# Performance work log

Hardware: AMD Instinct MI355X
Metric: run time of the kernel (lower is better)

Reference implementation:

```python
import jax, jax.numpy as jnp
import numpy as np
import math

B, N, D, H = 2, 64, 256, 8
DK = D // H


def setup_inputs() -> dict:
    key = jax.random.key(0)
    ks = jax.random.split(key, 12)
    s = 1.0 / math.sqrt(D)
    inp = {
        "state": jax.random.normal(ks[0], (B, N, N, D), dtype=jnp.float32),
        "mask": jnp.zeros((B, N, N, N), dtype=bool),
        "W_lk": jax.random.normal(ks[1], (D, D), dtype=jnp.float32) * s,
        "b_lk": jnp.zeros((D,), dtype=jnp.float32),
        "W_rk": jax.random.normal(ks[2], (D, D), dtype=jnp.float32) * s,
        "b_rk": jnp.zeros((D,), dtype=jnp.float32),
        "W_lv": jax.random.normal(ks[3], (D, D), dtype=jnp.float32) * s,
        "b_lv": jnp.zeros((D,), dtype=jnp.float32),
        "W_rv": jax.random.normal(ks[4], (D, D), dtype=jnp.float32) * s,
        "b_rv": jnp.zeros((D,), dtype=jnp.float32),
        "W_o": jax.random.normal(ks[5], (D, D), dtype=jnp.float32) * s,
        "b_o": jnp.zeros((D,), dtype=jnp.float32),
    }
    return inp


def _proj(x, W, b):
    # torch nn.Linear: x @ W.T + b, then view to heads
    y = jnp.einsum('bxyd,ed->bxye', x, W) + b
    return y.reshape(B, N, N, H, DK)


def reference(state, mask, W_lk, b_lk, W_rk, b_rk, W_lv, b_lv, W_rv, b_rv, W_o, b_o):
    left_k = _proj(state, W_lk, b_lk)   # [B,N,N,H,DK]
    right_k = _proj(state, W_rk, b_rk)
    left_v = _proj(state, W_lv, b_lv)
    right_v = _proj(state, W_rv, b_rv)

    # triangle-style scores over node triples (x, a, y): [B,N,N,N,H]
    scores = jnp.einsum('bxahd,bayhd->bxayh', left_k, right_k) / math.sqrt(DK)
    scores = jnp.where(mask[..., None], jnp.float32(-1000.0), scores)
    att = jax.nn.softmax(scores, axis=2)  # softmax over intermediate node a

    # val[b,x,a,y,h,d] = left_v[b,x,a,h,d] * right_v[b,a,y,h,d] (materialized as in torch)
    val = jnp.einsum('bxahd,bayhd->bxayhd', left_v, right_v)
    x = jnp.einsum('bxayh,bxayhd->bxyhd', att, val)  # sum over a
    x = x.reshape(B, N, N, D)
    return jnp.einsum('bxyd,ed->bxye', x, W_o) + b_o
```

## Files before the change

### kernel.cpp

```cpp
#include <hip/hip_runtime.h>

#define B 2
#define N 64
#define D 256
#define H 8
#define DK 32
#define M (B * N * N)

typedef __attribute__((ext_vector_type(8))) short bf16x8;
typedef __attribute__((ext_vector_type(4))) float f32x4;

#define PROJ_ELEMS (2097152)

__device__ __forceinline__ ushort f2b(float f) {
    union { float f; unsigned u; } v; v.f = f;
    unsigned r = v.u + 0x7fffu + ((v.u >> 16) & 1u);
    return (ushort)(r >> 16);
}
__device__ __forceinline__ float b2f(ushort u) {
    union { unsigned u; float f; } v; v.u = ((unsigned)u) << 16; return v.f;
}
__device__ __forceinline__ void cvt8(float4 raw, float* f) {
    const ushort* s = (const ushort*)&raw;
#pragma unroll
    for (int j = 0; j < 8; ++j) f[j] = b2f(s[j]);
}

__device__ __forceinline__ void glds16(const ushort* g, ushort* l) {
    __builtin_amdgcn_global_load_lds(
        (const __attribute__((address_space(1))) unsigned int*)g,
        (__attribute__((address_space(3))) unsigned int*)l, 16, 0, 0);
}

__global__ __launch_bounds__(256) void cast_all(const float* __restrict__ state,
                                                const float* __restrict__ W_lk, const float* __restrict__ W_rk,
                                                const float* __restrict__ W_lv, const float* __restrict__ W_rv,
                                                const float* __restrict__ W_o,
                                                const float* __restrict__ b_lk, const float* __restrict__ b_rk,
                                                const float* __restrict__ b_lv, const float* __restrict__ b_rv,
                                                const float* __restrict__ b_o,
                                                ushort* __restrict__ state_bf,
                                                ushort* __restrict__ Wcat,
                                                float* __restrict__ bias_cat) {
    const int gid = blockIdx.x * 256 + threadIdx.x;
    const float* Ws[5] = {W_lk, W_rk, W_lv, W_rv, W_o};
    const float* bs[5] = {b_lk, b_rk, b_lv, b_rv, b_o};

    if (gid < 1280) bias_cat[gid] = bs[gid >> 8][gid & 255];

    if (gid < 524288) {
        float4 v = *(const float4*)&state[(size_t)gid * 4];
        ushort4 o = {f2b(v.x), f2b(v.y), f2b(v.z), f2b(v.w)};
        *(ushort4*)&state_bf[(size_t)gid * 4] = o;
    } else {
        int u = gid - 524288;
        int row = u >> 6;
        int k4 = (u & 63) * 4;
        const float* W = Ws[row >> 8];
        float4 v = *(const float4*)&W[(size_t)(row & 255) * 256 + k4];
        ushort4 o = {f2b(v.x), f2b(v.y), f2b(v.z), f2b(v.w)};
        *(ushort4*)&Wcat[(size_t)row * 256 + k4] = o;
    }
}

template <int BF16OUT, int RELAYOUT>
__global__ __launch_bounds__(256) void gemm_mfma(const ushort* __restrict__ A,
                                                 const ushort* __restrict__ Bw,
                                                 const float* __restrict__ bias,
                                                 void* __restrict__ Cv, int ldc) {
    __shared__ __align__(16) ushort As[128 * 32];
    __shared__ __align__(16) ushort Bs[128 * 32];
    const int tid = threadIdx.x;
    const int lane = tid & 63;
    const int wave = tid >> 6;
    const int wm = (wave & 1) * 64;
    const int wn = (wave >> 1) * 64;
    const int row0 = blockIdx.x * 128;
    const int col0 = blockIdx.y * 128;

    const int lr = lane >> 2;
    const int lkq = (lane & 3) * 8;

    const ushort* gA0 = A + (size_t)(row0 + wave * 32 + lr) * 256 + lkq;
    const ushort* gA1 = gA0 + 16 * 256;
    const ushort* gB0 = Bw + (size_t)(col0 + wave * 32 + lr) * 256 + lkq;
    const ushort* gB1 = gB0 + 16 * 256;
    ushort* lA0 = &As[(wave * 32) * 32];
    ushort* lA1 = &As[(wave * 32 + 16) * 32];
    ushort* lB0 = &Bs[(wave * 32) * 32];
    ushort* lB1 = &Bs[(wave * 32 + 16) * 32];

    const int fr = lane & 15;
    const int fk = (lane >> 4) * 8;

    f32x4 acc[4][4] = {};

    for (int k0 = 0; k0 < 256; k0 += 32) {
        __syncthreads();
        glds16(gA0 + k0, lA0);
        glds16(gA1 + k0, lA1);
        glds16(gB0 + k0, lB0);
        glds16(gB1 + k0, lB1);
        __syncthreads();

        bf16x8 af[4], bf[4];
#pragma unroll
        for (int i = 0; i < 4; ++i)
            af[i] = *(const bf16x8*)&As[(wm + i * 16 + fr) * 32 + fk];
#pragma unroll
        for (int j = 0; j < 4; ++j)
            bf[j] = *(const bf16x8*)&Bs[(wn + j * 16 + fr) * 32 + fk];
#pragma unroll
        for (int i = 0; i < 4; ++i)
#pragma unroll
            for (int j = 0; j < 4; ++j)
                acc[i][j] = __builtin_amdgcn_mfma_f32_16x16x32_bf16(af[i], bf[j], acc[i][j], 0, 0, 0);
    }

#pragma unroll
    for (int j = 0; j < 4; ++j) {
        const int col = col0 + wn + j * 16 + (lane & 15);
        const float bv = bias[col];
#pragma unroll
        for (int i = 0; i < 4; ++i) {
            const int rbase = row0 + wm + i * 16 + (lane >> 4) * 4;
#pragma unroll
            for (int r = 0; r < 4; ++r) {
                float o = acc[i][j][r] + bv;
                if (RELAYOUT) {
                    const int row = rbase + r;
                    const int bb = row >> 12, rr = row & 4095;
                    const int proj = col >> 8, hh = (col >> 5) & 7, dk = col & 31;
                    ((ushort*)Cv)[(size_t)proj * PROJ_ELEMS +
                                  ((size_t)(bb * 8 + hh) * 4096 + rr) * 32 + dk] = f2b(o);
                } else if (BF16OUT) {
                    ((ushort*)Cv)[(size_t)(rbase + r) * ldc + col] = f2b(o);
                } else {
                    ((float*)Cv)[(size_t)(rbase + r) * ldc + col] = o;
                }
            }
        }
    }
}

__global__ __launch_bounds__(512) void fused_attn(const ushort* __restrict__ P,
                                                  const unsigned char* __restrict__ mask,
                                                  ushort* __restrict__ xbuf) {
    __shared__ __align__(16) float LVs[16 * 16 * 44];
    __shared__ __align__(16) float RVs[16 * 16 * 44];
    __shared__ __align__(16) float atts[16 * 16 * 20];
    __shared__ float mstate[16 * 20];
    __shared__ float lstate[16 * 20];
    __shared__ float alphas[16 * 20];

    const int bh = blockIdx.z;
    const int b = bh >> 3, h = bh & 7;
    const int x0 = blockIdx.x * 16, y0 = blockIdx.y * 16;
    const int tid = threadIdx.x;
    const int lane = tid & 63, wave = tid >> 6;

    const size_t HB = (size_t)bh * 4096 * 32;
    const ushort* PLK = P + HB;
    const ushort* PRK = P + (size_t)1 * PROJ_ELEMS + HB;
    const ushort* PLV = P + (size_t)2 * PROJ_ELEMS + HB;
    const ushort* PRV = P + (size_t)3 * PROJ_ELEMS + HB;

    const int y2 = (tid >> 4) & 3, dp = tid & 15;
    const int sx = tid >> 4, sy = tid & 15;
    if (tid < 256) {
        mstate[sx * 20 + sy] = -3.0e38f;
        lstate[sx * 20 + sy] = 0.0f;
    }

    float2 acc[2][4] = {};
    const float scale = 0.17677669529663687f;

    for (int ac = 0; ac < N; ac += 16) {
        __syncthreads();
#pragma unroll
        for (int it = 0; it < 2; ++it) {
            const int row = (tid >> 2) + it * 128;
            const int q = tid & 3;
            const int a = row >> 4, r = row & 15;
            float f[8];
            cvt8(*(const float4*)&PLV[((size_t)(x0 + r) * 64 + ac + a) * 32 + q * 8], f);
            *(float4*)&LVs[row * 44 + q * 8]     = make_float4(f[0], f[1], f[2], f[3]);
            *(float4*)&LVs[row * 44 + q * 8 + 4] = make_float4(f[4], f[5], f[6], f[7]);
            cvt8(*(const float4*)&PRV[((size_t)(ac + a) * 64 + y0 + r) * 32 + q * 8], f);
            *(float4*)&RVs[row * 44 + q * 8]     = make_float4(f[0], f[1], f[2], f[3]);
            *(float4*)&RVs[row * 44 + q * 8 + 4] = make_float4(f[4], f[5], f[6], f[7]);
        }
        {
            const int fr = lane & 15, fk = (lane >> 4) * 8;
            const int yq = lane & 15, xq = (lane >> 4) * 4;
#pragma unroll
            for (int aw = 0; aw < 2; ++aw) {
                const int a = wave * 2 + aw;
                bf16x8 af = *(const bf16x8*)&PLK[((size_t)(x0 + fr) * 64 + ac + a) * 32 + fk];
                bf16x8 bf = *(const bf16x8*)&PRK[((size_t)(ac + a) * 64 + y0 + fr) * 32 + fk];
                f32x4 s = {};
                s = __builtin_amdgcn_mfma_f32_16x16x32_bf16(af, bf, s, 0, 0, 0);
#pragma unroll
                for (int rr = 0; rr < 4; ++rr) {
                    const int x = xq + rr;
                    float sv = s[rr] * scale;
                    if (mask[((size_t)(b * N + x0 + x) * N + ac + a) * N + y0 + yq]) sv = -1000.0f;
                    atts[(a * 16 + x) * 20 + yq] = sv;
                }
            }
        }
        __syncthreads();

        if (tid < 256) {
            float s16[16];
            float mc = -3.0e38f;
#pragma unroll
            for (int a = 0; a < 16; ++a) {
                s16[a] = atts[(a * 16 + sx) * 20 + sy];
                mc = fmaxf(mc, s16[a]);
            }
            const float mold = mstate[sx * 20 + sy];
            const float mnew = fmaxf(mold, mc);
            const float alpha = __expf(mold - mnew);
            float ps = 0.0f;
#pragma unroll
            for (int a = 0; a < 16; ++a) {
                float p = __expf(s16[a] - mnew);
                atts[(a * 16 + sx) * 20 + sy] = p;
                ps += p;
            }
            lstate[sx * 20 + sy] = lstate[sx * 20 + sy] * alpha + ps;
            mstate[sx * 20 + sy] = mnew;
            alphas[sx * 20 + sy] = alpha;
        }
        __syncthreads();

#pragma unroll
        for (int i = 0; i < 2; ++i) {
            const int x = wave * 2 + i;
            float4 av = *(const float4*)&alphas[x * 20 + y2 * 4];
            const float* ap = (const float*)&av;
#pragma unroll
            for (int j = 0; j < 4; ++j) {
                acc[i][j].x *= ap[j];
                acc[i][j].y *= ap[j];
            }
        }
#pragma unroll
        for (int a = 0; a < 16; ++a) {
            float2 lv[2], rv[4];
#pragma unroll
            for (int i = 0; i < 2; ++i)
                lv[i] = *(const float2*)&LVs[(a * 16 + wave * 2 + i) * 44 + dp * 2];
#pragma unroll
            for (int j = 0; j < 4; ++j)
                rv[j] = *(const float2*)&RVs[(a * 16 + y2 * 4 + j) * 44 + dp * 2];
#pragma unroll
            for (int i = 0; i < 2; ++i) {
                float4 wv = *(const float4*)&atts[(a * 16 + wave * 2 + i) * 20 + y2 * 4];
                const float* wp = (const float*)&wv;
#pragma unroll
                for (int j = 0; j < 4; ++j) {
                    acc[i][j].x += (wp[j] * lv[i].x) * rv[j].x;
                    acc[i][j].y += (wp[j] * lv[i].y) * rv[j].y;
                }
            }
        }
    }

#pragma unroll
    for (int i = 0; i < 2; ++i) {
        const int x = wave * 2 + i;
        float4 lq = *(const float4*)&lstate[x * 20 + y2 * 4];
        const float* lp = (const float*)&lq;
#pragma unroll
        for (int j = 0; j < 4; ++j) {
            const float il = 1.0f / lp[j];
            ushort2 o = {f2b(acc[i][j].x * il), f2b(acc[i][j].y * il)};
            *(ushort2*)&xbuf[(((size_t)b * N + x0 + x) * N + y0 + y2 * 4 + j) * D + h * DK + 2 * dp] = o;
        }
    }
}

extern "C" void kernel_launch(void* const* d_in, const int* in_sizes, int n_in,
                              void* d_out, int out_size, void* d_ws, size_t ws_size,
                              hipStream_t stream) {
    const float* state = (const float*)d_in[0];
    const unsigned char* mask = (const unsigned char*)d_in[1];
    const float* W_lk = (const float*)d_in[2];
    const float* b_lk = (const float*)d_in[3];
    const float* W_rk = (const float*)d_in[4];
    const float* b_rk = (const float*)d_in[5];
    const float* W_lv = (const float*)d_in[6];
    const float* b_lv = (const float*)d_in[7];
    const float* W_rv = (const float*)d_in[8];
    const float* b_rv = (const float*)d_in[9];
    const float* W_o = (const float*)d_in[10];
    const float* b_o = (const float*)d_in[11];
    float* out = (float*)d_out;

    char* ws = (char*)d_ws;
    ushort* P_bf = (ushort*)ws;
    ws += (size_t)4 * PROJ_ELEMS * 2;
    float* bias_cat = (float*)ws;
    ws += 1280 * 4;
    ushort* state_bf = (ushort*)ws;
    ws += (size_t)M * D * 2;
    ushort* Wcat = (ushort*)ws;
    ws += (size_t)1280 * 256 * 2;
    ushort* xbuf_bf = (ushort*)ws;

    cast_all<<<2368, 256, 0, stream>>>(state, W_lk, W_rk, W_lv, W_rv, W_o,
                                       b_lk, b_rk, b_lv, b_rv, b_o,
                                       state_bf, Wcat, bias_cat);
    gemm_mfma<1, 1><<<dim3(M / 128, 8), 256, 0, stream>>>(state_bf, Wcat, bias_cat, P_bf, 1024);
    fused_attn<<<dim3(4, 4, B * H), 512, 0, stream>>>(P_bf, mask, xbuf_bf);
    gemm_mfma<0, 0><<<dim3(M / 128, 2), 256, 0, stream>>>(xbuf_bf, Wcat + 1024 * 256, bias_cat + 1024, out, 256);
}
```

Measured before the change: 124.5 us.

## Split fused attention across head-dim halves and keep V tiles in bf16 LDS

The fused attention kernel now launches twice as many blocks of 256 threads, each handling one half of the 32-wide head dimension, so 512 blocks are spread over the GPU instead of 256. The left and right value tiles are stored in LDS as raw bf16 and unpacked on read, which halves their shared memory and removes the conversion step at load time. The cost is that every block recomputes the full QK scores and softmax for its tile, doubling that work, plus extra unpacking instructions in the inner loop.

Measured after the change: 123.8 us. No clear change (-0.6%).

```diff
diff --git a/kernel.cpp b/kernel.cpp
--- a/kernel.cpp
+++ b/kernel.cpp
@@ -19,6 +19,12 @@
 }
 __device__ __forceinline__ float b2f(ushort u) {
     union { unsigned u; float f; } v; v.u = ((unsigned)u) << 16; return v.f;
+}
+__device__ __forceinline__ float2 up2(unsigned u) {
+    union { unsigned u; float f; } lo, hi;
+    lo.u = u << 16;
+    hi.u = u & 0xffff0000u;
+    return make_float2(lo.f, hi.f);
 }
 __device__ __forceinline__ void cvt8(float4 raw, float* f) {
     const ushort* s = (const ushort*)&raw;
@@ -143,17 +149,18 @@
     }
 }
 
-__global__ __launch_bounds__(512) void fused_attn(const ushort* __restrict__ P,
+__global__ __launch_bounds__(256) void fused_attn(const ushort* __restrict__ P,
                                                   const unsigned char* __restrict__ mask,
                                                   ushort* __restrict__ xbuf) {
-    __shared__ __align__(16) float LVs[16 * 16 * 44];
-    __shared__ __align__(16) float RVs[16 * 16 * 44];
-    __shared__ __align__(16) float atts[16 * 16 * 20];
+    __shared__ __align__(16) ushort LVs[256 * 24];
+    __shared__ __align__(16) ushort RVs[256 * 24];
+    __shared__ __align__(16) float atts[256 * 20];
     __shared__ float mstate[16 * 20];
     __shared__ float lstate[16 * 20];
     __shared__ float alphas[16 * 20];
 
-    const int bh = blockIdx.z;
+    const int bhz = blockIdx.z;
+    const int bh = bhz >> 1, dhalf = bhz & 1;
     const int b = bh >> 3, h = bh & 7;
     const int x0 = blockIdx.x * 16, y0 = blockIdx.y * 16;
     const int tid = threadIdx.x;
@@ -165,37 +172,31 @@
     const ushort* PLV = P + (size_t)2 * PROJ_ELEMS + HB;
     const ushort* PRV = P + (size_t)3 * PROJ_ELEMS + HB;
 
-    const int y2 = (tid >> 4) & 3, dp = tid & 15;
+    const int dp = tid & 7, y2 = (tid >> 3) & 3, xg = tid >> 5;
     const int sx = tid >> 4, sy = tid & 15;
-    if (tid < 256) {
-        mstate[sx * 20 + sy] = -3.0e38f;
-        lstate[sx * 20 + sy] = 0.0f;
-    }
+    mstate[sx * 20 + sy] = -3.0e38f;
+    lstate[sx * 20 + sy] = 0.0f;
 
     float2 acc[2][4] = {};
     const float scale = 0.17677669529663687f;
 
     for (int ac = 0; ac < N; ac += 16) {
         __syncthreads();
-#pragma unroll
-        for (int it = 0; it < 2; ++it) {
-            const int row = (tid >> 2) + it * 128;
-            const int q = tid & 3;
-            const int a = row >> 4, r = row & 15;
-            float f[8];
-            cvt8(*(const float4*)&PLV[((size_t)(x0 + r) * 64 + ac + a) * 32 + q * 8], f);
-            *(float4*)&LVs[row * 44 + q * 8]     = make_float4(f[0], f[1], f[2], f[3]);
-            *(float4*)&LVs[row * 44 + q * 8 + 4] = make_float4(f[4], f[5], f[6], f[7]);
-            cvt8(*(const float4*)&PRV[((size_t)(ac + a) * 64 + y0 + r) * 32 + q * 8], f);
-            *(float4*)&RVs[row * 44 + q * 8]     = make_float4(f[0], f[1], f[2], f[3]);
-            *(float4*)&RVs[row * 44 + q * 8 + 4] = make_float4(f[4], f[5], f[6], f[7]);
+        {
+            const int a = tid >> 4, r = tid & 15;
+            const ushort* s = &PLV[((size_t)(x0 + r) * 64 + ac + a) * 32 + dhalf * 16];
+            *(float4*)&LVs[tid * 24 + 0] = *(const float4*)&s[0];
+            *(float4*)&LVs[tid * 24 + 8] = *(const float4*)&s[8];
+            const ushort* s2 = &PRV[((size_t)(ac + a) * 64 + y0 + r) * 32 + dhalf * 16];
+            *(float4*)&RVs[tid * 24 + 0] = *(const float4*)&s2[0];
+            *(float4*)&RVs[tid * 24 + 8] = *(const float4*)&s2[8];
         }
         {
             const int fr = lane & 15, fk = (lane >> 4) * 8;
             const int yq = lane & 15, xq = (lane >> 4) * 4;
 #pragma unroll
-            for (int aw = 0; aw < 2; ++aw) {
-                const int a = wave * 2 + aw;
+            for (int aw = 0; aw < 4; ++aw) {
+                const int a = wave * 4 + aw;
                 bf16x8 af = *(const bf16x8*)&PLK[((size_t)(x0 + fr) * 64 + ac + a) * 32 + fk];
                 bf16x8 bf = *(const bf16x8*)&PRK[((size_t)(ac + a) * 64 + y0 + fr) * 32 + fk];
                 f32x4 s = {};
@@ -211,7 +212,7 @@
         }
         __syncthreads();
 
-        if (tid < 256) {
+        {
             float s16[16];
             float mc = -3.0e38f;
 #pragma unroll
@@ -237,8 +238,7 @@
 
 #pragma unroll
         for (int i = 0; i < 2; ++i) {
-            const int x = wave * 2 + i;
-            float4 av = *(const float4*)&alphas[x * 20 + y2 * 4];
+            float4 av = *(const float4*)&alphas[(xg * 2 + i) * 20 + y2 * 4];
             const float* ap = (const float*)&av;
 #pragma unroll
             for (int j = 0; j < 4; ++j) {
@@ -251,13 +251,13 @@
             float2 lv[2], rv[4];
 #pragma unroll
             for (int i = 0; i < 2; ++i)
-                lv[i] = *(const float2*)&LVs[(a * 16 + wave * 2 + i) * 44 + dp * 2];
+                lv[i] = up2(*(const unsigned*)&LVs[(a * 16 + xg * 2 + i) * 24 + dp * 2]);
 #pragma unroll
             for (int j = 0; j < 4; ++j)
-                rv[j] = *(const float2*)&RVs[(a * 16 + y2 * 4 + j) * 44 + dp * 2];
+                rv[j] = up2(*(const unsigned*)&RVs[(a * 16 + y2 * 4 + j) * 24 + dp * 2]);
 #pragma unroll
             for (int i = 0; i < 2; ++i) {
-                float4 wv = *(const float4*)&atts[(a * 16 + wave * 2 + i) * 20 + y2 * 4];
+                float4 wv = *(const float4*)&atts[(a * 16 + xg * 2 + i) * 20 + y2 * 4];
                 const float* wp = (const float*)&wv;
 #pragma unroll
                 for (int j = 0; j < 4; ++j) {
@@ -270,14 +270,15 @@
 
 #pragma unroll
     for (int i = 0; i < 2; ++i) {
-        const int x = wave * 2 + i;
+        const int x = xg * 2 + i;
         float4 lq = *(const float4*)&lstate[x * 20 + y2 * 4];
         const float* lp = (const float*)&lq;
 #pragma unroll
         for (int j = 0; j < 4; ++j) {
             const float il = 1.0f / lp[j];
             ushort2 o = {f2b(acc[i][j].x * il), f2b(acc[i][j].y * il)};
-            *(ushort2*)&xbuf[(((size_t)b * N + x0 + x) * N + y0 + y2 * 4 + j) * D + h * DK + 2 * dp] = o;
+            *(ushort2*)&xbuf[(((size_t)b * N + x0 + x) * N + y0 + y2 * 4 + j) * D +
+                             h * DK + dhalf * 16 + dp * 2] = o;
         }
     }
 }
@@ -314,6 +315,6 @@
                                        b_lk, b_rk, b_lv, b_rv, b_o,
                                        state_bf, Wcat, bias_cat);
     gemm_mfma<1, 1><<<dim3(M / 128, 8), 256, 0, stream>>>(state_bf, Wcat, bias_cat, P_bf, 1024);
-    fused_attn<<<dim3(4, 4, B * H), 512, 0, stream>>>(P_bf, mask, xbuf_bf);
+    fused_attn<<<dim3(4, 4, B * H * 2), 256, 0, stream>>>(P_bf, mask, xbuf_bf);
     gemm_mfma<0, 0><<<dim3(M / 128, 2), 256, 0, stream>>>(xbuf_bf, Wcat + 1024 * 256, bias_cat + 1024, out, 256);
 }
```
